# Kernel optimization log

Measured on AMD Instinct MI355X. Metric: run time of the kernel, lower is better.

## Reference

```python
import jax, jax.numpy as jnp
import numpy as np

TS = 4          # texture_size
S = 128         # image_size
DIST = 2.732    # neural_renderer default camera distance
EPS = 1e-9


def _grid_sample(img, grid):
    # img: (C,H,W); grid: (N,2) xy in [-1,1]. Bilinear, zero padding, align_corners=False
    C, H, W = img.shape
    x = (grid[:, 0] + 1.0) * (W * 0.5) - 0.5
    y = (grid[:, 1] + 1.0) * (H * 0.5) - 0.5
    x0 = jnp.floor(x)
    y0 = jnp.floor(y)
    tx = x - x0
    ty = y - y0

    def tap(xi, yi, w):
        valid = (xi >= 0) & (xi < W) & (yi >= 0) & (yi < H)
        xc = jnp.clip(xi, 0, W - 1).astype(jnp.int32)
        yc = jnp.clip(yi, 0, H - 1).astype(jnp.int32)
        return img[:, yc, xc] * jnp.where(valid, w, 0.0)[None]

    return (tap(x0, y0, (1 - tx) * (1 - ty)) + tap(x0 + 1, y0, tx * (1 - ty))
            + tap(x0, y0 + 1, (1 - tx) * ty) + tap(x0 + 1, y0 + 1, tx * ty))


def _look_at(v, eye):
    up = jnp.array([0.0, 1.0, 0.0], dtype=v.dtype)
    z = -eye / jnp.linalg.norm(eye)          # at = origin
    x = jnp.cross(up, z)
    x = x / jnp.linalg.norm(x)
    y = jnp.cross(z, x)
    y = y / jnp.linalg.norm(y)
    R = jnp.stack([x, y, z])                 # (3,3) rows = camera axes
    return (v - eye) @ R.T


def _forward(vertices, texture_image, texture_grid, faces, azi, ele):
    F = faces.shape[0]
    # --- texture resample (F.grid_sample) ---
    cols = _grid_sample(texture_image[0], texture_grid.reshape(-1, 2))  # (3, F*TS^3)
    textures = cols.T.reshape(F, TS, TS, TS, 3)

    # --- camera (orthographic look_at from elevation/azimuth, degrees) ---
    a = jnp.deg2rad(jnp.float32(azi))
    e = jnp.deg2rad(jnp.float32(ele))
    eye = DIST * jnp.stack([jnp.cos(e) * jnp.sin(a), jnp.sin(e), -jnp.cos(e) * jnp.cos(a)])
    v = _look_at(vertices, eye)              # (V,3)
    fv = v[faces]                            # (F,3,3)

    p0, p1, p2 = fv[:, 0, :2], fv[:, 1, :2], fv[:, 2, :2]
    e1 = p1 - p0
    e2 = p2 - p0
    det = e1[:, 0] * e2[:, 1] - e1[:, 1] * e2[:, 0]              # (F,)
    inv = 1.0 / jnp.where(jnp.abs(det) > EPS, det, 1.0)

    # pixel centers in NDC; row 0 = top (y=+1)
    xs = (jnp.arange(S) + 0.5) / S * 2.0 - 1.0
    ys = 1.0 - (jnp.arange(S) + 0.5) / S * 2.0
    px, py = jnp.meshgrid(xs, ys)            # (S,S)
    pix = jnp.stack([px.ravel(), py.ravel()], -1)                # (P,2), P=S*S

    d = pix[:, None, :] - p0[None]                               # (P,F,2)
    w1 = (d[..., 0] * e2[:, 1] - d[..., 1] * e2[:, 0]) * inv     # (P,F)
    w2 = (e1[:, 0] * d[..., 1] - e1[:, 1] * d[..., 0]) * inv
    w0 = 1.0 - w1 - w2
    inside = (w0 >= 0) & (w1 >= 0) & (w2 >= 0) & (jnp.abs(det) > EPS)[None]

    z = fv[:, :, 2]                                              # (F,3)
    depth = w0 * z[:, 0] + w1 * z[:, 1] + w2 * z[:, 2]
    depth = jnp.where(inside, depth, jnp.inf)
    fid = jnp.argmin(depth, axis=1)                              # (P,) nearest face (z-buffer)
    hit = jnp.isfinite(jnp.min(depth, axis=1))

    P = pix.shape[0]
    rows = jnp.arange(P)
    wb = jnp.stack([w0[rows, fid], w1[rows, fid], w2[rows, fid]], -1)   # (P,3) barycentrics
    idx = jnp.clip(jnp.floor(wb * TS).astype(jnp.int32), 0, TS - 1)     # nearest cell in TS^3 cube
    col = textures[fid, idx[:, 0], idx[:, 1], idx[:, 2]]                # (P,3)
    col = jnp.where(hit[:, None], col, 0.0)                             # black background

    img = col.reshape(S, S, 3).transpose(2, 0, 1)[None]                 # (1,3,S,S)
    return img[:, :, :, ::-1]                                           # torch.flip(images,[3])


def setup_inputs() -> dict:
    key = jax.random.key(0)
    k1, k2, k3, k4 = jax.random.split(key, 4)
    vertices = jax.random.uniform(k1, (1200, 3), minval=-0.9, maxval=0.9, dtype=jnp.float32)
    faces = jax.random.randint(k2, (2000, 3), 0, 1200, dtype=jnp.int32)
    texture_image = jax.random.uniform(k3, (1, 3, 512, 512), dtype=jnp.float32)
    texture_grid = jax.random.uniform(k4, (1, 2000 * TS ** 3, 2), minval=-1.0, maxval=1.0, dtype=jnp.float32)
    return {"vertices": vertices, "texture_image": texture_image,
            "texture_grid": texture_grid, "faces": faces, "azi": 180, "ele": 0}


def reference(vertices, texture_image, texture_grid, faces, azi, ele):
    return _forward(vertices, texture_image, texture_grid, faces, azi, ele)
```

## Files before the change

### kernel.cpp

```cpp
#include <hip/hip_runtime.h>
#include <math.h>

#define TS 4
#define SDIM 128
#define PIX (SDIM * SDIM)
#define TEXW 512
#define TEXH 512
#define EPS 1e-9f
#define NCHUNK 32
#define NTILE 64
#define BBOX_MARGIN 1e-3f

__device__ inline void cross3(const float a[3], const float b[3], float o[3]) {
    o[0] = a[1] * b[2] - a[2] * b[1];
    o[1] = a[2] * b[0] - a[0] * b[2];
    o[2] = a[0] * b[1] - a[1] * b[0];
}

__global__ void setup_kernel(const float* __restrict__ verts,
                             const int* __restrict__ faces,
                             const void* __restrict__ azi_p,
                             const void* __restrict__ ele_p,
                             float4* __restrict__ fd,
                             unsigned long long* __restrict__ zbuf,
                             int F, int faceBlocks) {
#pragma clang fp contract(off)
    if ((int)blockIdx.x >= faceBlocks) {
        int t = (blockIdx.x - faceBlocks) * 256 + threadIdx.x;
        if (t < PIX) zbuf[t] = ~0ull;
        return;
    }
    int f = blockIdx.x * 256 + threadIdx.x;
    if (f >= F) return;
    int ai = *(const int*)azi_p;
    float az = (ai > -360000 && ai < 360000) ? (float)ai : *(const float*)azi_p;
    int ei = *(const int*)ele_p;
    float el = (ei > -360000 && ei < 360000) ? (float)ei : *(const float*)ele_p;
    float a = az * (float)(M_PI / 180.0);
    float e = el * (float)(M_PI / 180.0);
    float ca = cosf(a), sa = sinf(a);
    float ce = cosf(e), se = sinf(e);
    float eye[3];
    eye[0] = 2.732f * (ce * sa);
    eye[1] = 2.732f * se;
    eye[2] = 2.732f * ((-ce) * ca);
    float nrm = sqrtf(eye[0] * eye[0] + eye[1] * eye[1] + eye[2] * eye[2]);
    float zv[3] = { (-eye[0]) / nrm, (-eye[1]) / nrm, (-eye[2]) / nrm };
    float up[3] = { 0.0f, 1.0f, 0.0f };
    float xv[3];
    cross3(up, zv, xv);
    float xn = sqrtf(xv[0] * xv[0] + xv[1] * xv[1] + xv[2] * xv[2]);
    xv[0] /= xn; xv[1] /= xn; xv[2] /= xn;
    float yv[3];
    cross3(zv, xv, yv);
    float yn = sqrtf(yv[0] * yv[0] + yv[1] * yv[1] + yv[2] * yv[2]);
    yv[0] /= yn; yv[1] /= yn; yv[2] /= yn;

    float q[3][3];
    for (int k = 0; k < 3; ++k) {
        int vi = faces[f * 3 + k];
        float d0 = verts[vi * 3 + 0] - eye[0];
        float d1 = verts[vi * 3 + 1] - eye[1];
        float d2 = verts[vi * 3 + 2] - eye[2];
        q[k][0] = d0 * xv[0] + d1 * xv[1] + d2 * xv[2];
        q[k][1] = d0 * yv[0] + d1 * yv[1] + d2 * yv[2];
        q[k][2] = d0 * zv[0] + d1 * zv[1] + d2 * zv[2];
    }
    float e1x = q[1][0] - q[0][0], e1y = q[1][1] - q[0][1];
    float e2x = q[2][0] - q[0][0], e2y = q[2][1] - q[0][1];
    float det = e1x * e2y - e1y * e2x;
    bool valid = fabsf(det) > EPS;
    float inv = 1.0f / (valid ? det : 1.0f);
    float z0 = valid ? q[0][2] : INFINITY;
    float z1 = valid ? q[1][2] : INFINITY;
    float z2 = valid ? q[2][2] : INFINITY;
    fd[f * 3 + 0] = make_float4(q[0][0], q[0][1], e1x, e1y);
    fd[f * 3 + 1] = make_float4(e2x, e2y, inv, 0.0f);
    fd[f * 3 + 2] = make_float4(z0, z1, z2, 0.0f);
}

__device__ inline unsigned int enc_depth(float d) {
    unsigned int u = __float_as_uint(d);
    return (u & 0x80000000u) ? ~u : (u | 0x80000000u);
}

__global__ void raster_kernel(const float4* __restrict__ fd, int F,
                              int chunkFaces,
                              unsigned long long* __restrict__ zbuf) {
#pragma clang fp contract(off)
    __shared__ float4 sfd[256 * 3];
    int tileX = blockIdx.x & 7, tileY = blockIdx.x >> 3;
    int f0 = blockIdx.y * chunkFaces;
    float xlo = (tileX * 16 + 0.5f) / 64.0f - 1.0f - BBOX_MARGIN;
    float xhi = (tileX * 16 + 15.5f) / 64.0f - 1.0f + BBOX_MARGIN;
    float yhi = 1.0f - (tileY * 16 + 0.5f) / 64.0f + BBOX_MARGIN;
    float ylo = 1.0f - (tileY * 16 + 15.5f) / 64.0f - BBOX_MARGIN;
    for (int k = threadIdx.x; k < chunkFaces; k += 256) {
        int f = f0 + k;
        float flag = 0.0f;
        float4 A, B, C;
        if (f < F) {
            A = fd[f * 3 + 0];
            B = fd[f * 3 + 1];
            C = fd[f * 3 + 2];
            float p1x = A.x + A.z, p1y = A.y + A.w;
            float p2x = A.x + B.x, p2y = A.y + B.y;
            float bxmin = fminf(A.x, fminf(p1x, p2x));
            float bxmax = fmaxf(A.x, fmaxf(p1x, p2x));
            float bymin = fminf(A.y, fminf(p1y, p2y));
            float bymax = fmaxf(A.y, fmaxf(p1y, p2y));
            if (bxmin <= xhi && bxmax >= xlo && bymin <= yhi && bymax >= ylo)
                flag = 1.0f;
        } else {
            A = make_float4(0.f, 0.f, 0.f, 0.f);
            B = make_float4(0.f, 0.f, 1.f, 0.f);
            C = make_float4(0.f, 0.f, 0.f, 0.f);
        }
        B.w = flag;
        sfd[k * 3 + 0] = A;
        sfd[k * 3 + 1] = B;
        sfd[k * 3 + 2] = C;
    }
    __syncthreads();
    int j = tileX * 16 + (threadIdx.x & 15);
    int i = tileY * 16 + (threadIdx.x >> 4);
    float px = ((j + 0.5f) / 128.0f) * 2.0f - 1.0f;
    float py = 1.0f - ((i + 0.5f) / 128.0f) * 2.0f;
    float best = INFINITY;
    int bfid = 0x7fffffff;
    bool have = false;
    for (int k = 0; k < chunkFaces; ++k) {
        float4 B = sfd[k * 3 + 1];
        if (B.w == 0.0f) continue;
        float4 A = sfd[k * 3 + 0];
        float4 C = sfd[k * 3 + 2];
        float dx = px - A.x, dy = py - A.y;
        float w1 = (dx * B.y - dy * B.x) * B.z;
        float w2 = (A.z * dy - A.w * dx) * B.z;
        float w0 = 1.0f - w1 - w2;
        bool inside = (w0 >= 0.0f) && (w1 >= 0.0f) && (w2 >= 0.0f);
        float depth = w0 * C.x + w1 * C.y + w2 * C.z;
        int f = f0 + k;
        if (inside && depth < INFINITY &&
            (depth < best || (depth == best && f < bfid))) {
            best = depth;
            bfid = f;
            have = true;
        }
    }
    if (have) {
        unsigned long long pack =
            ((unsigned long long)enc_depth(best) << 32) | (unsigned int)bfid;
        atomicMin(&zbuf[i * SDIM + j], pack);
    }
}

__global__ void shade_kernel(const unsigned long long* __restrict__ zbuf,
                             const float4* __restrict__ fd,
                             const float* __restrict__ img,
                             const float* __restrict__ grid,
                             float* __restrict__ out) {
#pragma clang fp contract(off)
    int t = blockIdx.x * 256 + threadIdx.x;
    int i = t >> 7, j = t & 127;
    int o = i * SDIM + (SDIM - 1 - j);
    unsigned long long pack = zbuf[t];
    if (pack == ~0ull) {
        out[0 * PIX + o] = 0.0f;
        out[1 * PIX + o] = 0.0f;
        out[2 * PIX + o] = 0.0f;
        return;
    }
    int bfid = (int)(unsigned int)(pack & 0xffffffffu);
    float4 A = fd[bfid * 3 + 0];
    float4 B = fd[bfid * 3 + 1];
    float px = ((j + 0.5f) / 128.0f) * 2.0f - 1.0f;
    float py = 1.0f - ((i + 0.5f) / 128.0f) * 2.0f;
    float dx = px - A.x, dy = py - A.y;
    float w1 = (dx * B.y - dy * B.x) * B.z;
    float w2 = (A.z * dy - A.w * dx) * B.z;
    float w0 = 1.0f - w1 - w2;
    int i0 = min(max((int)floorf(w0 * (float)TS), 0), TS - 1);
    int i1 = min(max((int)floorf(w1 * (float)TS), 0), TS - 1);
    int i2 = min(max((int)floorf(w2 * (float)TS), 0), TS - 1);
    int sidx = bfid * (TS * TS * TS) + i0 * 16 + i1 * 4 + i2;
    float gx = grid[2 * sidx], gy = grid[2 * sidx + 1];
    float x = (gx + 1.0f) * (TEXW * 0.5f) - 0.5f;
    float y = (gy + 1.0f) * (TEXH * 0.5f) - 0.5f;
    float x0f = floorf(x), y0f = floorf(y);
    float tx = x - x0f, ty = y - y0f;
    int x0 = (int)x0f, y0 = (int)y0f;
    float w00 = (1.0f - tx) * (1.0f - ty);
    float w10 = tx * (1.0f - ty);
    float w01 = (1.0f - tx) * ty;
    float w11 = tx * ty;
    bool vx0 = (x0 >= 0) && (x0 < TEXW);
    bool vx1 = (x0 + 1 >= 0) && (x0 + 1 < TEXW);
    bool vy0 = (y0 >= 0) && (y0 < TEXH);
    bool vy1 = (y0 + 1 >= 0) && (y0 + 1 < TEXH);
    int xc0 = min(max(x0, 0), TEXW - 1);
    int xc1 = min(max(x0 + 1, 0), TEXW - 1);
    int yc0 = min(max(y0, 0), TEXH - 1);
    int yc1 = min(max(y0 + 1, 0), TEXH - 1);
    float W00 = (vx0 && vy0) ? w00 : 0.0f;
    float W10 = (vx1 && vy0) ? w10 : 0.0f;
    float W01 = (vx0 && vy1) ? w01 : 0.0f;
    float W11 = (vx1 && vy1) ? w11 : 0.0f;
    for (int c = 0; c < 3; ++c) {
        const float* ic = img + c * (TEXH * TEXW);
        float acc = ic[yc0 * TEXW + xc0] * W00;
        acc = acc + ic[yc0 * TEXW + xc1] * W10;
        acc = acc + ic[yc1 * TEXW + xc0] * W01;
        acc = acc + ic[yc1 * TEXW + xc1] * W11;
        out[c * PIX + o] = acc;
    }
}

extern "C" void kernel_launch(void* const* d_in, const int* in_sizes, int n_in,
                              void* d_out, int out_size, void* d_ws,
                              size_t ws_size, hipStream_t stream) {
    const float* verts = (const float*)d_in[0];
    const float* img = (const float*)d_in[1];
    const float* grid = (const float*)d_in[2];
    const int* faces = (const int*)d_in[3];
    const void* azi = d_in[4];
    const void* ele = d_in[5];
    float* out = (float*)d_out;

    int F = in_sizes[3] / 3;

    char* ws = (char*)d_ws;
    size_t off = 0;
    float4* fd = (float4*)(ws + off);
    off += ((size_t)F * 3 * 16 + 255) & ~(size_t)255;
    unsigned long long* zbuf = (unsigned long long*)(ws + off);

    int faceBlocks = (F + 255) / 256;
    int zBlocks = (PIX + 255) / 256;
    int chunkFaces = (F + NCHUNK - 1) / NCHUNK;

    setup_kernel<<<faceBlocks + zBlocks, 256, 0, stream>>>(
        verts, faces, azi, ele, fd, zbuf, F, faceBlocks);
    raster_kernel<<<dim3(NTILE, NCHUNK), 256, 0, stream>>>(fd, F, chunkFaces,
                                                           zbuf);
    shade_kernel<<<PIX / 256, 256, 0, stream>>>(zbuf, fd, img, grid, out);
}
```

Baseline: 91.83 us.

## Fuse face setup into raster, compact faces per tile, replace atomic zbuffer with partials

Removes the separate setup kernel by having each raster block recompute the camera and transform its chunk's faces, compacting bbox-overlapping faces into shared memory via a counter so the inner loop skips culled entries. Per-chunk depth/face partials are written instead of 64-bit atomicMin on a cleared z-buffer, and the shade kernel reduces across chunks and recomputes the winning face's geometry. This cuts one launch and the zbuf clear, at the cost of redundant camera/face math and a 32-way reduction read in shading. MAXCF=128 caps chunk size, which is sufficient for F=2000 but would silently drop faces for larger meshes.

After: 94.69 us. 3.1% more time.

```diff
diff --git a/kernel.cpp b/kernel.cpp
--- a/kernel.cpp
+++ b/kernel.cpp
@@ -9,29 +9,14 @@
 #define EPS 1e-9f
 #define NCHUNK 32
 #define NTILE 64
+#define MAXCF 128
 #define BBOX_MARGIN 1e-3f
 
-__device__ inline void cross3(const float a[3], const float b[3], float o[3]) {
-    o[0] = a[1] * b[2] - a[2] * b[1];
-    o[1] = a[2] * b[0] - a[0] * b[2];
-    o[2] = a[0] * b[1] - a[1] * b[0];
-}
-
-__global__ void setup_kernel(const float* __restrict__ verts,
-                             const int* __restrict__ faces,
-                             const void* __restrict__ azi_p,
-                             const void* __restrict__ ele_p,
-                             float4* __restrict__ fd,
-                             unsigned long long* __restrict__ zbuf,
-                             int F, int faceBlocks) {
-#pragma clang fp contract(off)
-    if ((int)blockIdx.x >= faceBlocks) {
-        int t = (blockIdx.x - faceBlocks) * 256 + threadIdx.x;
-        if (t < PIX) zbuf[t] = ~0ull;
-        return;
-    }
-    int f = blockIdx.x * 256 + threadIdx.x;
-    if (f >= F) return;
+__device__ __forceinline__ void camera_setup(const void* azi_p,
+                                             const void* ele_p, float eye[3],
+                                             float xv[3], float yv[3],
+                                             float zv[3]) {
+#pragma clang fp contract(off)
     int ai = *(const int*)azi_p;
     float az = (ai > -360000 && ai < 360000) ? (float)ai : *(const float*)azi_p;
     int ei = *(const int*)ele_p;
@@ -40,23 +25,30 @@
     float e = el * (float)(M_PI / 180.0);
     float ca = cosf(a), sa = sinf(a);
     float ce = cosf(e), se = sinf(e);
-    float eye[3];
     eye[0] = 2.732f * (ce * sa);
     eye[1] = 2.732f * se;
     eye[2] = 2.732f * ((-ce) * ca);
     float nrm = sqrtf(eye[0] * eye[0] + eye[1] * eye[1] + eye[2] * eye[2]);
-    float zv[3] = { (-eye[0]) / nrm, (-eye[1]) / nrm, (-eye[2]) / nrm };
-    float up[3] = { 0.0f, 1.0f, 0.0f };
-    float xv[3];
-    cross3(up, zv, xv);
-    float xn = sqrtf(xv[0] * xv[0] + xv[1] * xv[1] + xv[2] * xv[2]);
-    xv[0] /= xn; xv[1] /= xn; xv[2] /= xn;
-    float yv[3];
-    cross3(zv, xv, yv);
-    float yn = sqrtf(yv[0] * yv[0] + yv[1] * yv[1] + yv[2] * yv[2]);
-    yv[0] /= yn; yv[1] /= yn; yv[2] /= yn;
-
-    float q[3][3];
+    zv[0] = (-eye[0]) / nrm;
+    zv[1] = (-eye[1]) / nrm;
+    zv[2] = (-eye[2]) / nrm;
+    float cx0 = 1.0f * zv[2] - 0.0f * zv[1];
+    float cx1 = 0.0f * zv[0] - 0.0f * zv[2];
+    float cx2 = 0.0f * zv[1] - 1.0f * zv[0];
+    float xn = sqrtf(cx0 * cx0 + cx1 * cx1 + cx2 * cx2);
+    xv[0] = cx0 / xn; xv[1] = cx1 / xn; xv[2] = cx2 / xn;
+    float cy0 = zv[1] * xv[2] - zv[2] * xv[1];
+    float cy1 = zv[2] * xv[0] - zv[0] * xv[2];
+    float cy2 = zv[0] * xv[1] - zv[1] * xv[0];
+    float yn = sqrtf(cy0 * cy0 + cy1 * cy1 + cy2 * cy2);
+    yv[0] = cy0 / yn; yv[1] = cy1 / yn; yv[2] = cy2 / yn;
+}
+
+__device__ __forceinline__ void face_transform(
+    const float* __restrict__ verts, const int* __restrict__ faces, int f,
+    const float eye[3], const float xv[3], const float yv[3],
+    const float zv[3], float q[3][3]) {
+#pragma clang fp contract(off)
     for (int k = 0; k < 3; ++k) {
         int vi = faces[f * 3 + k];
         float d0 = verts[vi * 3 + 0] - eye[0];
@@ -66,119 +58,131 @@
         q[k][1] = d0 * yv[0] + d1 * yv[1] + d2 * yv[2];
         q[k][2] = d0 * zv[0] + d1 * zv[1] + d2 * zv[2];
     }
-    float e1x = q[1][0] - q[0][0], e1y = q[1][1] - q[0][1];
-    float e2x = q[2][0] - q[0][0], e2y = q[2][1] - q[0][1];
-    float det = e1x * e2y - e1y * e2x;
-    bool valid = fabsf(det) > EPS;
-    float inv = 1.0f / (valid ? det : 1.0f);
-    float z0 = valid ? q[0][2] : INFINITY;
-    float z1 = valid ? q[1][2] : INFINITY;
-    float z2 = valid ? q[2][2] : INFINITY;
-    fd[f * 3 + 0] = make_float4(q[0][0], q[0][1], e1x, e1y);
-    fd[f * 3 + 1] = make_float4(e2x, e2y, inv, 0.0f);
-    fd[f * 3 + 2] = make_float4(z0, z1, z2, 0.0f);
-}
-
-__device__ inline unsigned int enc_depth(float d) {
-    unsigned int u = __float_as_uint(d);
-    return (u & 0x80000000u) ? ~u : (u | 0x80000000u);
-}
-
-__global__ void raster_kernel(const float4* __restrict__ fd, int F,
-                              int chunkFaces,
-                              unsigned long long* __restrict__ zbuf) {
-#pragma clang fp contract(off)
-    __shared__ float4 sfd[256 * 3];
+}
+
+__global__ void raster_kernel(const float* __restrict__ verts,
+                              const int* __restrict__ faces,
+                              const void* __restrict__ azi_p,
+                              const void* __restrict__ ele_p,
+                              uint2* __restrict__ partial, int F,
+                              int chunkFaces) {
+#pragma clang fp contract(off)
+    __shared__ float4 sA[MAXCF];
+    __shared__ float4 sB[MAXCF];
+    __shared__ float4 sZ[MAXCF];
+    __shared__ int cnt;
+    if (threadIdx.x == 0) cnt = 0;
+    __syncthreads();
+
     int tileX = blockIdx.x & 7, tileY = blockIdx.x >> 3;
-    int f0 = blockIdx.y * chunkFaces;
+    int chunk = blockIdx.y;
+    int f0 = chunk * chunkFaces;
     float xlo = (tileX * 16 + 0.5f) / 64.0f - 1.0f - BBOX_MARGIN;
     float xhi = (tileX * 16 + 15.5f) / 64.0f - 1.0f + BBOX_MARGIN;
     float yhi = 1.0f - (tileY * 16 + 0.5f) / 64.0f + BBOX_MARGIN;
     float ylo = 1.0f - (tileY * 16 + 15.5f) / 64.0f - BBOX_MARGIN;
-    for (int k = threadIdx.x; k < chunkFaces; k += 256) {
-        int f = f0 + k;
-        float flag = 0.0f;
-        float4 A, B, C;
-        if (f < F) {
-            A = fd[f * 3 + 0];
-            B = fd[f * 3 + 1];
-            C = fd[f * 3 + 2];
-            float p1x = A.x + A.z, p1y = A.y + A.w;
-            float p2x = A.x + B.x, p2y = A.y + B.y;
-            float bxmin = fminf(A.x, fminf(p1x, p2x));
-            float bxmax = fmaxf(A.x, fmaxf(p1x, p2x));
-            float bymin = fminf(A.y, fminf(p1y, p2y));
-            float bymax = fmaxf(A.y, fmaxf(p1y, p2y));
-            if (bxmin <= xhi && bxmax >= xlo && bymin <= yhi && bymax >= ylo)
-                flag = 1.0f;
-        } else {
-            A = make_float4(0.f, 0.f, 0.f, 0.f);
-            B = make_float4(0.f, 0.f, 1.f, 0.f);
-            C = make_float4(0.f, 0.f, 0.f, 0.f);
+
+    float eye[3], xv[3], yv[3], zv[3];
+    camera_setup(azi_p, ele_p, eye, xv, yv, zv);
+
+    int k = threadIdx.x;
+    int f = f0 + k;
+    if (k < chunkFaces && k < MAXCF && f < F) {
+        float q[3][3];
+        face_transform(verts, faces, f, eye, xv, yv, zv, q);
+        float e1x = q[1][0] - q[0][0], e1y = q[1][1] - q[0][1];
+        float e2x = q[2][0] - q[0][0], e2y = q[2][1] - q[0][1];
+        float det = e1x * e2y - e1y * e2x;
+        bool valid = fabsf(det) > EPS;
+        float inv = 1.0f / (valid ? det : 1.0f);
+        float z0 = valid ? q[0][2] : INFINITY;
+        float z1 = valid ? q[1][2] : INFINITY;
+        float z2 = valid ? q[2][2] : INFINITY;
+        float p1x = q[0][0] + e1x, p1y = q[0][1] + e1y;
+        float p2x = q[0][0] + e2x, p2y = q[0][1] + e2y;
+        float bxmin = fminf(q[0][0], fminf(p1x, p2x));
+        float bxmax = fmaxf(q[0][0], fmaxf(p1x, p2x));
+        float bymin = fminf(q[0][1], fminf(p1y, p2y));
+        float bymax = fmaxf(q[0][1], fmaxf(p1y, p2y));
+        if (bxmin <= xhi && bxmax >= xlo && bymin <= yhi && bymax >= ylo) {
+            int pos = atomicAdd(&cnt, 1);
+            sA[pos] = make_float4(q[0][0], q[0][1], e1x, e1y);
+            sB[pos] = make_float4(e2x, e2y, inv, __int_as_float(f));
+            sZ[pos] = make_float4(z0, z1, z2, 0.0f);
         }
-        B.w = flag;
-        sfd[k * 3 + 0] = A;
-        sfd[k * 3 + 1] = B;
-        sfd[k * 3 + 2] = C;
     }
     __syncthreads();
+    int n = cnt;
+
     int j = tileX * 16 + (threadIdx.x & 15);
     int i = tileY * 16 + (threadIdx.x >> 4);
     float px = ((j + 0.5f) / 128.0f) * 2.0f - 1.0f;
     float py = 1.0f - ((i + 0.5f) / 128.0f) * 2.0f;
     float best = INFINITY;
     int bfid = 0x7fffffff;
-    bool have = false;
-    for (int k = 0; k < chunkFaces; ++k) {
-        float4 B = sfd[k * 3 + 1];
-        if (B.w == 0.0f) continue;
-        float4 A = sfd[k * 3 + 0];
-        float4 C = sfd[k * 3 + 2];
+    for (int s = 0; s < n; ++s) {
+        float4 A = sA[s];
+        float4 B = sB[s];
+        float4 C = sZ[s];
         float dx = px - A.x, dy = py - A.y;
         float w1 = (dx * B.y - dy * B.x) * B.z;
         float w2 = (A.z * dy - A.w * dx) * B.z;
         float w0 = 1.0f - w1 - w2;
         bool inside = (w0 >= 0.0f) && (w1 >= 0.0f) && (w2 >= 0.0f);
         float depth = w0 * C.x + w1 * C.y + w2 * C.z;
-        int f = f0 + k;
+        int fid = __float_as_int(B.w);
         if (inside && depth < INFINITY &&
-            (depth < best || (depth == best && f < bfid))) {
+            (depth < best || (depth == best && fid < bfid))) {
             best = depth;
-            bfid = f;
-            have = true;
+            bfid = fid;
         }
     }
-    if (have) {
-        unsigned long long pack =
-            ((unsigned long long)enc_depth(best) << 32) | (unsigned int)bfid;
-        atomicMin(&zbuf[i * SDIM + j], pack);
-    }
-}
-
-__global__ void shade_kernel(const unsigned long long* __restrict__ zbuf,
-                             const float4* __restrict__ fd,
+    partial[chunk * PIX + i * SDIM + j] =
+        make_uint2(__float_as_uint(best), (unsigned int)bfid);
+}
+
+__global__ void shade_kernel(const uint2* __restrict__ partial,
+                             const float* __restrict__ verts,
+                             const int* __restrict__ faces,
+                             const void* __restrict__ azi_p,
+                             const void* __restrict__ ele_p,
                              const float* __restrict__ img,
                              const float* __restrict__ grid,
-                             float* __restrict__ out) {
+                             float* __restrict__ out, int nChunks) {
 #pragma clang fp contract(off)
     int t = blockIdx.x * 256 + threadIdx.x;
     int i = t >> 7, j = t & 127;
     int o = i * SDIM + (SDIM - 1 - j);
-    unsigned long long pack = zbuf[t];
-    if (pack == ~0ull) {
+    float best = INFINITY;
+    int bfid = 0x7fffffff;
+    for (int c = 0; c < nChunks; ++c) {
+        uint2 P = partial[c * PIX + t];
+        float d = __uint_as_float(P.x);
+        int fid = (int)P.y;
+        if (d < best || (d == best && fid < bfid)) {
+            best = d;
+            bfid = fid;
+        }
+    }
+    if (!isfinite(best)) {
         out[0 * PIX + o] = 0.0f;
         out[1 * PIX + o] = 0.0f;
         out[2 * PIX + o] = 0.0f;
         return;
     }
-    int bfid = (int)(unsigned int)(pack & 0xffffffffu);
-    float4 A = fd[bfid * 3 + 0];
-    float4 B = fd[bfid * 3 + 1];
+    float eye[3], xv[3], yv[3], zv[3];
+    camera_setup(azi_p, ele_p, eye, xv, yv, zv);
+    float q[3][3];
+    face_transform(verts, faces, bfid, eye, xv, yv, zv, q);
+    float e1x = q[1][0] - q[0][0], e1y = q[1][1] - q[0][1];
+    float e2x = q[2][0] - q[0][0], e2y = q[2][1] - q[0][1];
+    float det = e1x * e2y - e1y * e2x;
+    float inv = 1.0f / (fabsf(det) > EPS ? det : 1.0f);
     float px = ((j + 0.5f) / 128.0f) * 2.0f - 1.0f;
     float py = 1.0f - ((i + 0.5f) / 128.0f) * 2.0f;
-    float dx = px - A.x, dy = py - A.y;
-    float w1 = (dx * B.y - dy * B.x) * B.z;
-    float w2 = (A.z * dy - A.w * dx) * B.z;
+    float dx = px - q[0][0], dy = py - q[0][1];
+    float w1 = (dx * e2y - dy * e2x) * inv;
+    float w2 = (e1x * dy - e1y * dx) * inv;
     float w0 = 1.0f - w1 - w2;
     int i0 = min(max((int)floorf(w0 * (float)TS), 0), TS - 1);
     int i1 = min(max((int)floorf(w1 * (float)TS), 0), TS - 1);
@@ -228,20 +232,12 @@
     float* out = (float*)d_out;
 
     int F = in_sizes[3] / 3;
-
-    char* ws = (char*)d_ws;
-    size_t off = 0;
-    float4* fd = (float4*)(ws + off);
-    off += ((size_t)F * 3 * 16 + 255) & ~(size_t)255;
-    unsigned long long* zbuf = (unsigned long long*)(ws + off);
-
-    int faceBlocks = (F + 255) / 256;
-    int zBlocks = (PIX + 255) / 256;
+    uint2* partial = (uint2*)d_ws;
+
     int chunkFaces = (F + NCHUNK - 1) / NCHUNK;
 
-    setup_kernel<<<faceBlocks + zBlocks, 256, 0, stream>>>(
-        verts, faces, azi, ele, fd, zbuf, F, faceBlocks);
-    raster_kernel<<<dim3(NTILE, NCHUNK), 256, 0, stream>>>(fd, F, chunkFaces,
-                                                           zbuf);
-    shade_kernel<<<PIX / 256, 256, 0, stream>>>(zbuf, fd, img, grid, out);
-}
+    raster_kernel<<<dim3(NTILE, NCHUNK), 256, 0, stream>>>(
+        verts, faces, azi, ele, partial, F, chunkFaces);
+    shade_kernel<<<PIX / 256, 256, 0, stream>>>(partial, verts, faces, azi,
+                                                ele, img, grid, out, NCHUNK);
+}
```
